# Performance work log

Hardware: AMD Instinct MI355X
Metric: run time of the kernel (lower is better)

The kernel has to match this reference:

```python
import jax, jax.numpy as jnp
import numpy as np

D_MODEL = 256
N_HEAD = 8


def quick_gelu(x):
    return x * jax.nn.sigmoid(1.702 * x)


def setup_inputs() -> dict:
    key = jax.random.key(0)
    ks = jax.random.split(key, 7)
    d = D_MODEL
    s = 0.02
    return {
        "x": jax.random.normal(ks[0], (2, 512, d), dtype=jnp.float32),
        "W_qkv": jax.random.normal(ks[1], (d, 3 * d), dtype=jnp.float32) * s,
        "b_qkv": jnp.zeros((3 * d,), dtype=jnp.float32),
        "W_fc": jax.random.normal(ks[2], (d, 4 * d), dtype=jnp.float32) * s,
        "b_fc": jnp.zeros((4 * d,), dtype=jnp.float32),
        "W_proj": jax.random.normal(ks[3], (4 * d, d), dtype=jnp.float32) * s,
        "b_proj": jnp.zeros((d,), dtype=jnp.float32),
    }


def attention_l1(x, W_qkv, b_qkv):
    bs, n_ctx, width = x.shape
    h = N_HEAD
    c = width // h
    scale = 1.0 / jnp.sqrt(jnp.asarray(c, x.dtype))
    qkv = (x @ W_qkv + b_qkv).reshape(bs, n_ctx, h, 3 * c)
    q, k, v = jnp.split(qkv, 3, axis=-1)  # each (b, t, h, c)
    qh = q.transpose(0, 2, 1, 3)  # (b, h, t, c)
    kh = k.transpose(0, 2, 1, 3)  # (b, h, s, c)
    vh = v.transpose(0, 2, 1, 3)  # (b, h, s, c)
    # L1 distance: sum_c |q - k| * scale  -> (b, h, t, s)
    dist = jnp.sum(jnp.abs(qh[:, :, :, None, :] - kh[:, :, None, :, :]), axis=-1) * scale
    weight = 1.0 / (0.001 + dist)
    idx = jnp.arange(n_ctx)
    weight = weight.at[:, :, idx, idx].set(0.0)
    wdtype = weight.dtype
    weight = jax.nn.softmax(weight.astype(jnp.float32), axis=-1).astype(wdtype)
    out = jnp.einsum('bhts,bhsc->bthc', weight, vh)
    return out.reshape(bs, n_ctx, width)


def reference(x, W_qkv, b_qkv, W_fc, b_fc, W_proj, b_proj):
    x = x + attention_l1(x, W_qkv, b_qkv)
    h = quick_gelu(x @ W_fc + b_fc)
    x = x + (h @ W_proj + b_proj)
    return x
```

## Files before the change

### kernel.cpp

```cpp
#include <hip/hip_runtime.h>
#include <hip/hip_bf16.h>
#include <hip/hip_fp16.h>

#define DM   256
#define NH   8
#define HC   32
#define SEQ  512
#define MTOT 1024

#define B_X1   0
#define B_QH   (1u<<20)
#define B_KH   0x180000u
#define B_VT   0x200000u
#define B_WFCT 0x280000u
#define B_WPJT 0x300000u

typedef __attribute__((ext_vector_type(8))) __bf16 bf16x8;
typedef __attribute__((ext_vector_type(4))) __bf16 bf16x4;
typedef __attribute__((ext_vector_type(4))) float  f32x4;

__device__ __forceinline__ float qgelu(float x) {
    return x / (1.0f + __expf(-1.702f * x));
}

#define BKP 264

__global__ __launch_bounds__(256)
void qkv_k(const float* __restrict__ x, const float* __restrict__ W,
           const float* __restrict__ bias,
           const float* __restrict__ Wfc, const float* __restrict__ Wproj,
           char* __restrict__ wsb)
{
    __shared__ float lt[64 * 65];
    __shared__ __align__(16) __bf16 lbt[16 * BKP];
    const int bid = blockIdx.x, tid = threadIdx.x;

    if (bid >= 768) {
        const int tt = bid - 768;
        const float* src; __bf16* dst; int K, N, tile;
        if (tt < 64) { src = Wfc;   dst = (__bf16*)(wsb + B_WFCT); K = 256;  N = 1024; tile = tt; }
        else         { src = Wproj; dst = (__bf16*)(wsb + B_WPJT); K = 1024; N = 256;  tile = tt - 64; }
        const int nn = N >> 6;
        const int k0 = (tile / nn) * 64, n0 = (tile % nn) * 64;
        const int rr0 = tid >> 4, c4 = tid & 15;
        #pragma unroll
        for (int i = 0; i < 4; ++i) {
            const int rr = rr0 + i * 16;
            float4 v = *(const float4*)&src[(size_t)(k0 + rr) * N + n0 + c4 * 4];
            lt[rr * 65 + c4 * 4 + 0] = v.x; lt[rr * 65 + c4 * 4 + 1] = v.y;
            lt[rr * 65 + c4 * 4 + 2] = v.z; lt[rr * 65 + c4 * 4 + 3] = v.w;
        }
        __syncthreads();
        #pragma unroll
        for (int i = 0; i < 4; ++i) {
            const int rr = rr0 + i * 16;
            bf16x4 b;
            b.x = (__bf16)lt[(c4 * 4 + 0) * 65 + rr];
            b.y = (__bf16)lt[(c4 * 4 + 1) * 65 + rr];
            b.z = (__bf16)lt[(c4 * 4 + 2) * 65 + rr];
            b.w = (__bf16)lt[(c4 * 4 + 3) * 65 + rr];
            *(bf16x4*)&dst[(size_t)(n0 + rr) * K + k0 + c4 * 4] = b;
        }
        return;
    }

    const int lane = tid & 63, wv = tid >> 6;
    const int n0 = (bid >> 4) * 16;
    const int m0 = ((bid * 4 + wv) & 63) * 16;
    const int r = lane & 15, q = lane >> 4;

    {
        const int kk = tid >> 2;
        const int c4 = (tid & 3) * 4;
        #pragma unroll
        for (int p = 0; p < 4; ++p) {
            const int k = p * 64 + kk;
            float4 w = *(const float4*)&W[(size_t)k * 768 + n0 + c4];
            lbt[(c4 + 0) * BKP + k] = (__bf16)w.x;
            lbt[(c4 + 1) * BKP + k] = (__bf16)w.y;
            lbt[(c4 + 2) * BKP + k] = (__bf16)w.z;
            lbt[(c4 + 3) * BKP + k] = (__bf16)w.w;
        }
    }
    __syncthreads();

    const float*  ap = x + (size_t)(m0 + r) * DM + q * 8;
    const __bf16* bl = &lbt[r * BKP + q * 8];

    f32x4 acc = {0.f, 0.f, 0.f, 0.f};
    #pragma unroll
    for (int kt = 0; kt < DM; kt += 32) {
        float4 a0 = *(const float4*)(ap + kt);
        float4 a1 = *(const float4*)(ap + kt + 4);
        bf16x8 af;
        af[0] = (__bf16)a0.x; af[1] = (__bf16)a0.y; af[2] = (__bf16)a0.z; af[3] = (__bf16)a0.w;
        af[4] = (__bf16)a1.x; af[5] = (__bf16)a1.y; af[6] = (__bf16)a1.z; af[7] = (__bf16)a1.w;
        bf16x8 bf = *(const bf16x8*)(bl + kt);
        acc = __builtin_amdgcn_mfma_f32_16x16x32_bf16(af, bf, acc, 0, 0, 0);
    }

    __half*  qh  = (__half*)(wsb + B_QH);
    __half*  kh  = (__half*)(wsb + B_KH);
    __bf16*  vtb = (__bf16*)(wsb + B_VT);
    const int n = n0 + r;
    const float bn = bias[n];
    const int h = n / 96, jj = n % 96;
    #pragma unroll
    for (int i = 0; i < 4; ++i) {
        const int m = m0 + q * 4 + i;
        const float v = acc[i] + bn;
        const int b = m >> 9, t = m & 511;
        const int bh = b * NH + h;
        if (jj < 32)      qh[((size_t)(bh * SEQ + t)) * HC + jj]        = (__half)v;
        else if (jj < 64) kh[((size_t)(bh * SEQ + t)) * HC + (jj - 32)] = (__half)v;
        else              vtb[((size_t)(bh * HC + (jj - 64))) * SEQ + t] = (__bf16)v;
    }
}

#define QT 16
#define PSTRIDE 514

__global__ __launch_bounds__(512, 4)
void attn_k(const char* __restrict__ wsb, const float* __restrict__ xin,
            float* __restrict__ x1, const float* __restrict__ bproj,
            float* __restrict__ out)
{
    __shared__ __half2 qtile[QT * 16];
    __shared__ __bf16  pmat[QT * PSTRIDE];
    __shared__ float   psum[QT * 8];
    __shared__ float   pinv[QT];

    const __half*  qhg = (const __half*)(wsb + B_QH);
    const __half*  khg = (const __half*)(wsb + B_KH);
    const __bf16*  vtb = (const __bf16*)(wsb + B_VT);

    const int tid  = threadIdx.x;
    const int lane = tid & 63;
    const int wv   = tid >> 6;
    const int sg   = tid;
    const int bh   = blockIdx.x >> 5;
    const int qbase = (blockIdx.x & 31) * QT;
    const float scale = 0.17677669529663687f;

    const __half2* kp = (const __half2*)(khg + ((size_t)(bh * SEQ + sg)) * HC);
    __half2 kr[16];
    #pragma unroll
    for (int j = 0; j < 16; ++j) kr[j] = kp[j];

    if (tid < 256) {
        const int t = tid >> 4, j = tid & 15;
        qtile[t * 16 + j] =
            *(const __half2*)(qhg + ((size_t)(bh * SEQ + qbase + t)) * HC + j * 2);
    }
    __syncthreads();

    #pragma unroll 4
    for (int t = 0; t < QT; ++t) {
        __half2 acc2 = __floats2half2_rn(0.f, 0.f);
        #pragma unroll
        for (int j = 0; j < 16; ++j) {
            __half2 dif = __hsub2(kr[j], qtile[t * 16 + j]);
            unsigned u = (*(unsigned*)&dif) & 0x7FFF7FFFu;
            acc2 = __hadd2(acc2, *(__half2*)&u);
        }
        const float d = __low2float(acc2) + __high2float(acc2);
        float w = 1.0f / (0.001f + d * scale);
        if (sg == qbase + t) w = 0.0f;
        float p = __expf(w);
        float se = p;
        #pragma unroll
        for (int off = 32; off >= 1; off >>= 1) se += __shfl_xor(se, off, 64);
        pmat[t * PSTRIDE + sg] = (__bf16)p;
        if (lane == 0) psum[t * 8 + wv] = se;
    }
    __syncthreads();

    if (tid < QT) {
        float s = 0.f;
        #pragma unroll
        for (int j = 0; j < 8; ++j) s += psum[tid * 8 + j];
        pinv[tid] = 1.0f / s;
    }
    __syncthreads();

    if (wv < 2) {
        const int r = lane & 15, q = lane >> 4;
        const __bf16* bp  = vtb + ((size_t)(bh * HC + wv * 16 + r)) * SEQ + q * 8;
        const __bf16* apm = &pmat[r * PSTRIDE + q * 8];
        f32x4 acc = {0.f, 0.f, 0.f, 0.f};
        #pragma unroll
        for (int kt = 0; kt < SEQ; kt += 32) {
            bf16x8 af = *(const bf16x8*)(apm + kt);
            bf16x8 bf = *(const bf16x8*)(bp + kt);
            acc = __builtin_amdgcn_mfma_f32_16x16x32_bf16(af, bf, acc, 0, 0, 0);
        }
        const int b = bh >> 3, hh = bh & 7;
        const int c = wv * 16 + r;
        const int col = hh * HC + c;
        const float bpn = bproj[col];
        #pragma unroll
        for (int i = 0; i < 4; ++i) {
            const int tl = q * 4 + i;
            const int t  = qbase + tl;
            const float v = acc[i] * pinv[tl];
            const int idx = ((b * SEQ + t) * DM) + col;
            const float res = xin[idx] + v;
            x1[idx]  = res;
            out[idx] = res + bpn;
        }
    }
}

#define HSTR 264

__global__ __launch_bounds__(512)
void mlp_k(const float* __restrict__ X1, const char* __restrict__ wsb,
           const float* __restrict__ bfc, float* __restrict__ out)
{
    __shared__ __align__(16) __bf16 hs[16 * HSTR];
    const __bf16* Wf = (const __bf16*)(wsb + B_WFCT);
    const __bf16* Wp = (const __bf16*)(wsb + B_WPJT);

    const int tid  = threadIdx.x;
    const int lane = tid & 63;
    const int wv   = tid >> 6;
    const int mt   = blockIdx.x & 63;
    const int ns   = blockIdx.x >> 6;
    const int m0   = mt * 16;
    const int r    = lane & 15, q = lane >> 4;

    {
        const float* ap = X1 + (size_t)(m0 + r) * DM + q * 8;
        f32x4 acc[2] = {};
        #pragma unroll
        for (int kt = 0; kt < DM; kt += 32) {
            float4 a0 = *(const float4*)(ap + kt);
            float4 a1 = *(const float4*)(ap + kt + 4);
            bf16x8 af;
            af[0] = (__bf16)a0.x; af[1] = (__bf16)a0.y; af[2] = (__bf16)a0.z; af[3] = (__bf16)a0.w;
            af[4] = (__bf16)a1.x; af[5] = (__bf16)a1.y; af[6] = (__bf16)a1.z; af[7] = (__bf16)a1.w;
            #pragma unroll
            for (int nt = 0; nt < 2; ++nt) {
                const int n0 = ns * 256 + (wv * 2 + nt) * 16;
                bf16x8 bf = *(const bf16x8*)(Wf + (size_t)(n0 + r) * DM + q * 8 + kt);
                acc[nt] = __builtin_amdgcn_mfma_f32_16x16x32_bf16(af, bf, acc[nt], 0, 0, 0);
            }
        }
        #pragma unroll
        for (int nt = 0; nt < 2; ++nt) {
            const int nl = (wv * 2 + nt) * 16 + r;
            const float bn = bfc[ns * 256 + nl];
            #pragma unroll
            for (int i = 0; i < 4; ++i)
                hs[(q * 4 + i) * HSTR + nl] = (__bf16)qgelu(acc[nt][i] + bn);
        }
    }
    __syncthreads();

    {
        f32x4 acc[2] = {};
        const __bf16* al = &hs[r * HSTR + q * 8];
        #pragma unroll
        for (int kt = 0; kt < 256; kt += 32) {
            bf16x8 af = *(const bf16x8*)(al + kt);
            #pragma unroll
            for (int nt = 0; nt < 2; ++nt) {
                const int n0 = wv * 32 + nt * 16;
                bf16x8 bf = *(const bf16x8*)(Wp + (size_t)(n0 + r) * 1024 +
                                             ns * 256 + q * 8 + kt);
                acc[nt] = __builtin_amdgcn_mfma_f32_16x16x32_bf16(af, bf, acc[nt], 0, 0, 0);
            }
        }
        #pragma unroll
        for (int nt = 0; nt < 2; ++nt) {
            const int n = wv * 32 + nt * 16 + r;
            #pragma unroll
            for (int i = 0; i < 4; ++i) {
                const int m = m0 + q * 4 + i;
                atomicAdd(&out[(size_t)m * DM + n], acc[nt][i]);
            }
        }
    }
}

extern "C" void kernel_launch(void* const* d_in, const int* in_sizes, int n_in,
                              void* d_out, int out_size, void* d_ws, size_t ws_size,
                              hipStream_t stream)
{
    (void)in_sizes; (void)n_in; (void)out_size; (void)ws_size;
    const float* x     = (const float*)d_in[0];
    const float* Wqkv  = (const float*)d_in[1];
    const float* bqkv  = (const float*)d_in[2];
    const float* Wfc   = (const float*)d_in[3];
    const float* bfc   = (const float*)d_in[4];
    const float* Wproj = (const float*)d_in[5];
    const float* bproj = (const float*)d_in[6];
    float* out = (float*)d_out;
    char*  wsb = (char*)d_ws;
    float* x1  = (float*)(wsb + B_X1);

    qkv_k<<<896, 256, 0, stream>>>(x, Wqkv, bqkv, Wfc, Wproj, wsb);

    attn_k<<<512, 512, 0, stream>>>(wsb, x, x1, bproj, out);

    mlp_k<<<256, 512, 0, stream>>>(x1, wsb, bfc, out);
}
```

Before: 106.8 us.

## Fuse QKV, attention and MLP kernels into one persistent kernel with grid barriers

Replaces three kernel launches with a single 256-block persistent kernel that runs the QKV GEMM and weight transposes, the L1 attention, and the MLP in phases. The phases are separated by atomic-counter grid barriers, and a memset resets the counter before each launch. Attention now handles 32 query rows per block instead of 16 so that 256 blocks cover the work. This removes launch gaps between kernels, but adds barrier spin cost, halves the number of attention blocks, and depends on all 256 blocks being co-resident.

```diff
diff --git a/kernel.cpp b/kernel.cpp
--- a/kernel.cpp
+++ b/kernel.cpp
@@ -14,6 +14,7 @@
 #define B_VT   0x200000u
 #define B_WFCT 0x280000u
 #define B_WPJT 0x300000u
+#define B_BAR  0x3C0000u
 
 typedef __attribute__((ext_vector_type(8))) __bf16 bf16x8;
 typedef __attribute__((ext_vector_type(4))) __bf16 bf16x4;
@@ -23,261 +24,283 @@
     return x / (1.0f + __expf(-1.702f * x));
 }
 
-#define BKP 264
-
-__global__ __launch_bounds__(256)
-void qkv_k(const float* __restrict__ x, const float* __restrict__ W,
-           const float* __restrict__ bias,
-           const float* __restrict__ Wfc, const float* __restrict__ Wproj,
-           char* __restrict__ wsb)
-{
-    __shared__ float lt[64 * 65];
-    __shared__ __align__(16) __bf16 lbt[16 * BKP];
-    const int bid = blockIdx.x, tid = threadIdx.x;
-
-    if (bid >= 768) {
-        const int tt = bid - 768;
-        const float* src; __bf16* dst; int K, N, tile;
-        if (tt < 64) { src = Wfc;   dst = (__bf16*)(wsb + B_WFCT); K = 256;  N = 1024; tile = tt; }
-        else         { src = Wproj; dst = (__bf16*)(wsb + B_WPJT); K = 1024; N = 256;  tile = tt - 64; }
-        const int nn = N >> 6;
-        const int k0 = (tile / nn) * 64, n0 = (tile % nn) * 64;
-        const int rr0 = tid >> 4, c4 = tid & 15;
-        #pragma unroll
-        for (int i = 0; i < 4; ++i) {
-            const int rr = rr0 + i * 16;
-            float4 v = *(const float4*)&src[(size_t)(k0 + rr) * N + n0 + c4 * 4];
-            lt[rr * 65 + c4 * 4 + 0] = v.x; lt[rr * 65 + c4 * 4 + 1] = v.y;
-            lt[rr * 65 + c4 * 4 + 2] = v.z; lt[rr * 65 + c4 * 4 + 3] = v.w;
-        }
-        __syncthreads();
-        #pragma unroll
-        for (int i = 0; i < 4; ++i) {
-            const int rr = rr0 + i * 16;
-            bf16x4 b;
-            b.x = (__bf16)lt[(c4 * 4 + 0) * 65 + rr];
-            b.y = (__bf16)lt[(c4 * 4 + 1) * 65 + rr];
-            b.z = (__bf16)lt[(c4 * 4 + 2) * 65 + rr];
-            b.w = (__bf16)lt[(c4 * 4 + 3) * 65 + rr];
-            *(bf16x4*)&dst[(size_t)(n0 + rr) * K + k0 + c4 * 4] = b;
-        }
-        return;
-    }
-
-    const int lane = tid & 63, wv = tid >> 6;
-    const int n0 = (bid >> 4) * 16;
-    const int m0 = ((bid * 4 + wv) & 63) * 16;
-    const int r = lane & 15, q = lane >> 4;
-
-    {
-        const int kk = tid >> 2;
-        const int c4 = (tid & 3) * 4;
-        #pragma unroll
-        for (int p = 0; p < 4; ++p) {
-            const int k = p * 64 + kk;
-            float4 w = *(const float4*)&W[(size_t)k * 768 + n0 + c4];
-            lbt[(c4 + 0) * BKP + k] = (__bf16)w.x;
-            lbt[(c4 + 1) * BKP + k] = (__bf16)w.y;
-            lbt[(c4 + 2) * BKP + k] = (__bf16)w.z;
-            lbt[(c4 + 3) * BKP + k] = (__bf16)w.w;
-        }
+#define NBLK    256
+#define BKP     264
+#define QT      32
+#define PSTRIDE 514
+#define HSTR    264
+
+__device__ __forceinline__ void gbar(unsigned* bar, unsigned target) {
+    __syncthreads();
+    if (threadIdx.x == 0) {
+        __threadfence();
+        __hip_atomic_fetch_add(bar, 1u, __ATOMIC_RELEASE, __HIP_MEMORY_SCOPE_AGENT);
+        while (__hip_atomic_load(bar, __ATOMIC_ACQUIRE, __HIP_MEMORY_SCOPE_AGENT) < target)
+            __builtin_amdgcn_s_sleep(2);
+        __threadfence();
     }
     __syncthreads();
-
-    const float*  ap = x + (size_t)(m0 + r) * DM + q * 8;
-    const __bf16* bl = &lbt[r * BKP + q * 8];
-
-    f32x4 acc = {0.f, 0.f, 0.f, 0.f};
-    #pragma unroll
-    for (int kt = 0; kt < DM; kt += 32) {
-        float4 a0 = *(const float4*)(ap + kt);
-        float4 a1 = *(const float4*)(ap + kt + 4);
-        bf16x8 af;
-        af[0] = (__bf16)a0.x; af[1] = (__bf16)a0.y; af[2] = (__bf16)a0.z; af[3] = (__bf16)a0.w;
-        af[4] = (__bf16)a1.x; af[5] = (__bf16)a1.y; af[6] = (__bf16)a1.z; af[7] = (__bf16)a1.w;
-        bf16x8 bf = *(const bf16x8*)(bl + kt);
-        acc = __builtin_amdgcn_mfma_f32_16x16x32_bf16(af, bf, acc, 0, 0, 0);
-    }
-
-    __half*  qh  = (__half*)(wsb + B_QH);
-    __half*  kh  = (__half*)(wsb + B_KH);
+}
+
+__global__ __launch_bounds__(512)
+void fused_k(const float* __restrict__ x, const float* __restrict__ W,
+             const float* __restrict__ bias,
+             const float* __restrict__ Wfc, const float* __restrict__ Wproj,
+             const float* __restrict__ bfc, const float* __restrict__ bproj,
+             char* __restrict__ wsb, float* __restrict__ out)
+{
+    __shared__ __align__(16) unsigned char SM[37 * 1024];
+    const int tid = threadIdx.x;
+    const int bid = blockIdx.x;
+    unsigned* bar = (unsigned*)(wsb + B_BAR);
+
+    float* x1 = (float*)(wsb + B_X1);
+    __half*  qhg = (__half*)(wsb + B_QH);
+    __half*  khg = (__half*)(wsb + B_KH);
     __bf16*  vtb = (__bf16*)(wsb + B_VT);
-    const int n = n0 + r;
-    const float bn = bias[n];
-    const int h = n / 96, jj = n % 96;
-    #pragma unroll
-    for (int i = 0; i < 4; ++i) {
-        const int m = m0 + q * 4 + i;
-        const float v = acc[i] + bn;
-        const int b = m >> 9, t = m & 511;
-        const int bh = b * NH + h;
-        if (jj < 32)      qh[((size_t)(bh * SEQ + t)) * HC + jj]        = (__half)v;
-        else if (jj < 64) kh[((size_t)(bh * SEQ + t)) * HC + (jj - 32)] = (__half)v;
-        else              vtb[((size_t)(bh * HC + (jj - 64))) * SEQ + t] = (__bf16)v;
-    }
-}
-
-#define QT 16
-#define PSTRIDE 514
-
-__global__ __launch_bounds__(512, 4)
-void attn_k(const char* __restrict__ wsb, const float* __restrict__ xin,
-            float* __restrict__ x1, const float* __restrict__ bproj,
-            float* __restrict__ out)
-{
-    __shared__ __half2 qtile[QT * 16];
-    __shared__ __bf16  pmat[QT * PSTRIDE];
-    __shared__ float   psum[QT * 8];
-    __shared__ float   pinv[QT];
-
-    const __half*  qhg = (const __half*)(wsb + B_QH);
-    const __half*  khg = (const __half*)(wsb + B_KH);
-    const __bf16*  vtb = (const __bf16*)(wsb + B_VT);
-
-    const int tid  = threadIdx.x;
-    const int lane = tid & 63;
-    const int wv   = tid >> 6;
-    const int sg   = tid;
-    const int bh   = blockIdx.x >> 5;
-    const int qbase = (blockIdx.x & 31) * QT;
-    const float scale = 0.17677669529663687f;
-
-    const __half2* kp = (const __half2*)(khg + ((size_t)(bh * SEQ + sg)) * HC);
-    __half2 kr[16];
-    #pragma unroll
-    for (int j = 0; j < 16; ++j) kr[j] = kp[j];
-
-    if (tid < 256) {
-        const int t = tid >> 4, j = tid & 15;
-        qtile[t * 16 + j] =
-            *(const __half2*)(qhg + ((size_t)(bh * SEQ + qbase + t)) * HC + j * 2);
-    }
-    __syncthreads();
-
-    #pragma unroll 4
-    for (int t = 0; t < QT; ++t) {
-        __half2 acc2 = __floats2half2_rn(0.f, 0.f);
-        #pragma unroll
-        for (int j = 0; j < 16; ++j) {
-            __half2 dif = __hsub2(kr[j], qtile[t * 16 + j]);
-            unsigned u = (*(unsigned*)&dif) & 0x7FFF7FFFu;
-            acc2 = __hadd2(acc2, *(__half2*)&u);
-        }
-        const float d = __low2float(acc2) + __high2float(acc2);
-        float w = 1.0f / (0.001f + d * scale);
-        if (sg == qbase + t) w = 0.0f;
-        float p = __expf(w);
-        float se = p;
-        #pragma unroll
-        for (int off = 32; off >= 1; off >>= 1) se += __shfl_xor(se, off, 64);
-        pmat[t * PSTRIDE + sg] = (__bf16)p;
-        if (lane == 0) psum[t * 8 + wv] = se;
-    }
-    __syncthreads();
-
-    if (tid < QT) {
-        float s = 0.f;
-        #pragma unroll
-        for (int j = 0; j < 8; ++j) s += psum[tid * 8 + j];
-        pinv[tid] = 1.0f / s;
-    }
-    __syncthreads();
-
-    if (wv < 2) {
-        const int r = lane & 15, q = lane >> 4;
-        const __bf16* bp  = vtb + ((size_t)(bh * HC + wv * 16 + r)) * SEQ + q * 8;
-        const __bf16* apm = &pmat[r * PSTRIDE + q * 8];
-        f32x4 acc = {0.f, 0.f, 0.f, 0.f};
-        #pragma unroll
-        for (int kt = 0; kt < SEQ; kt += 32) {
-            bf16x8 af = *(const bf16x8*)(apm + kt);
-            bf16x8 bf = *(const bf16x8*)(bp + kt);
-            acc = __builtin_amdgcn_mfma_f32_16x16x32_bf16(af, bf, acc, 0, 0, 0);
-        }
-        const int b = bh >> 3, hh = bh & 7;
-        const int c = wv * 16 + r;
-        const int col = hh * HC + c;
-        const float bpn = bproj[col];
-        #pragma unroll
-        for (int i = 0; i < 4; ++i) {
-            const int tl = q * 4 + i;
-            const int t  = qbase + tl;
-            const float v = acc[i] * pinv[tl];
-            const int idx = ((b * SEQ + t) * DM) + col;
-            const float res = xin[idx] + v;
-            x1[idx]  = res;
-            out[idx] = res + bpn;
-        }
-    }
-}
-
-#define HSTR 264
-
-__global__ __launch_bounds__(512)
-void mlp_k(const float* __restrict__ X1, const char* __restrict__ wsb,
-           const float* __restrict__ bfc, float* __restrict__ out)
-{
-    __shared__ __align__(16) __bf16 hs[16 * HSTR];
-    const __bf16* Wf = (const __bf16*)(wsb + B_WFCT);
-    const __bf16* Wp = (const __bf16*)(wsb + B_WPJT);
-
-    const int tid  = threadIdx.x;
-    const int lane = tid & 63;
-    const int wv   = tid >> 6;
-    const int mt   = blockIdx.x & 63;
-    const int ns   = blockIdx.x >> 6;
-    const int m0   = mt * 16;
-    const int r    = lane & 15, q = lane >> 4;
-
-    {
-        const float* ap = X1 + (size_t)(m0 + r) * DM + q * 8;
-        f32x4 acc[2] = {};
-        #pragma unroll
-        for (int kt = 0; kt < DM; kt += 32) {
-            float4 a0 = *(const float4*)(ap + kt);
-            float4 a1 = *(const float4*)(ap + kt + 4);
-            bf16x8 af;
-            af[0] = (__bf16)a0.x; af[1] = (__bf16)a0.y; af[2] = (__bf16)a0.z; af[3] = (__bf16)a0.w;
-            af[4] = (__bf16)a1.x; af[5] = (__bf16)a1.y; af[6] = (__bf16)a1.z; af[7] = (__bf16)a1.w;
-            #pragma unroll
-            for (int nt = 0; nt < 2; ++nt) {
-                const int n0 = ns * 256 + (wv * 2 + nt) * 16;
-                bf16x8 bf = *(const bf16x8*)(Wf + (size_t)(n0 + r) * DM + q * 8 + kt);
-                acc[nt] = __builtin_amdgcn_mfma_f32_16x16x32_bf16(af, bf, acc[nt], 0, 0, 0);
-            }
-        }
-        #pragma unroll
-        for (int nt = 0; nt < 2; ++nt) {
-            const int nl = (wv * 2 + nt) * 16 + r;
-            const float bn = bfc[ns * 256 + nl];
-            #pragma unroll
-            for (int i = 0; i < 4; ++i)
-                hs[(q * 4 + i) * HSTR + nl] = (__bf16)qgelu(acc[nt][i] + bn);
-        }
-    }
-    __syncthreads();
-
-    {
-        f32x4 acc[2] = {};
-        const __bf16* al = &hs[r * HSTR + q * 8];
-        #pragma unroll
-        for (int kt = 0; kt < 256; kt += 32) {
-            bf16x8 af = *(const bf16x8*)(al + kt);
-            #pragma unroll
-            for (int nt = 0; nt < 2; ++nt) {
-                const int n0 = wv * 32 + nt * 16;
-                bf16x8 bf = *(const bf16x8*)(Wp + (size_t)(n0 + r) * 1024 +
-                                             ns * 256 + q * 8 + kt);
-                acc[nt] = __builtin_amdgcn_mfma_f32_16x16x32_bf16(af, bf, acc[nt], 0, 0, 0);
-            }
-        }
-        #pragma unroll
-        for (int nt = 0; nt < 2; ++nt) {
-            const int n = wv * 32 + nt * 16 + r;
+
+    for (int pass = 0; pass < 2; ++pass) {
+        const int sub = tid >> 8;
+        const int vt  = tid & 255;
+        const int vb  = pass * 512 + bid * 2 + sub;
+        unsigned char* SB = SM + sub * 16640;
+        float*  lt  = (float*)SB;
+        __bf16* lbt = (__bf16*)SB;
+
+        const bool gemm = (vb < 768);
+        const bool tp   = (vb >= 768) && (vb < 896);
+
+        if (gemm) {
+            const int n0 = (vb >> 4) * 16;
+            const int kk = vt >> 2, c4 = (vt & 3) * 4;
+            #pragma unroll
+            for (int p = 0; p < 4; ++p) {
+                const int k = p * 64 + kk;
+                float4 w = *(const float4*)&W[(size_t)k * 768 + n0 + c4];
+                lbt[(c4 + 0) * BKP + k] = (__bf16)w.x;
+                lbt[(c4 + 1) * BKP + k] = (__bf16)w.y;
+                lbt[(c4 + 2) * BKP + k] = (__bf16)w.z;
+                lbt[(c4 + 3) * BKP + k] = (__bf16)w.w;
+            }
+        } else if (tp) {
+            const int tt = vb - 768;
+            const float* src; int K, N, tile;
+            if (tt < 64) { src = Wfc;   K = 256;  N = 1024; tile = tt; }
+            else         { src = Wproj; K = 1024; N = 256;  tile = tt - 64; }
+            const int nn = N >> 6;
+            const int k0 = (tile / nn) * 64, n0t = (tile % nn) * 64;
+            const int rr0 = vt >> 4, c4 = vt & 15;
+            #pragma unroll
+            for (int i = 0; i < 4; ++i) {
+                const int rr = rr0 + i * 16;
+                float4 v = *(const float4*)&src[(size_t)(k0 + rr) * N + n0t + c4 * 4];
+                lt[rr * 65 + c4 * 4 + 0] = v.x; lt[rr * 65 + c4 * 4 + 1] = v.y;
+                lt[rr * 65 + c4 * 4 + 2] = v.z; lt[rr * 65 + c4 * 4 + 3] = v.w;
+            }
+        }
+        __syncthreads();
+
+        if (gemm) {
+            const int lane = vt & 63, wv = vt >> 6;
+            const int n0 = (vb >> 4) * 16;
+            const int m0 = ((vb * 4 + wv) & 63) * 16;
+            const int r = lane & 15, q = lane >> 4;
+            const float*  ap = x + (size_t)(m0 + r) * DM + q * 8;
+            const __bf16* bl = &lbt[r * BKP + q * 8];
+            f32x4 acc = {0.f, 0.f, 0.f, 0.f};
+            #pragma unroll
+            for (int kt = 0; kt < DM; kt += 32) {
+                float4 a0 = *(const float4*)(ap + kt);
+                float4 a1 = *(const float4*)(ap + kt + 4);
+                bf16x8 af;
+                af[0] = (__bf16)a0.x; af[1] = (__bf16)a0.y; af[2] = (__bf16)a0.z; af[3] = (__bf16)a0.w;
+                af[4] = (__bf16)a1.x; af[5] = (__bf16)a1.y; af[6] = (__bf16)a1.z; af[7] = (__bf16)a1.w;
+                bf16x8 bf = *(const bf16x8*)(bl + kt);
+                acc = __builtin_amdgcn_mfma_f32_16x16x32_bf16(af, bf, acc, 0, 0, 0);
+            }
+            const int n = n0 + r;
+            const float bn = bias[n];
+            const int h = n / 96, jj = n % 96;
             #pragma unroll
             for (int i = 0; i < 4; ++i) {
                 const int m = m0 + q * 4 + i;
-                atomicAdd(&out[(size_t)m * DM + n], acc[nt][i]);
+                const float v = acc[i] + bn;
+                const int b = m >> 9, t = m & 511;
+                const int bh = b * NH + h;
+                if (jj < 32)      qhg[((size_t)(bh * SEQ + t)) * HC + jj]        = (__half)v;
+                else if (jj < 64) khg[((size_t)(bh * SEQ + t)) * HC + (jj - 32)] = (__half)v;
+                else              vtb[((size_t)(bh * HC + (jj - 64))) * SEQ + t] = (__bf16)v;
+            }
+        } else if (tp) {
+            const int tt = vb - 768;
+            __bf16* dst; int K, N, tile;
+            if (tt < 64) { dst = (__bf16*)(wsb + B_WFCT); K = 256;  N = 1024; tile = tt; }
+            else         { dst = (__bf16*)(wsb + B_WPJT); K = 1024; N = 256;  tile = tt - 64; }
+            const int nn = N >> 6;
+            const int k0 = (tile / nn) * 64, n0t = (tile % nn) * 64;
+            const int rr0 = vt >> 4, c4 = vt & 15;
+            #pragma unroll
+            for (int i = 0; i < 4; ++i) {
+                const int rr = rr0 + i * 16;
+                bf16x4 bv;
+                bv.x = (__bf16)lt[(c4 * 4 + 0) * 65 + rr];
+                bv.y = (__bf16)lt[(c4 * 4 + 1) * 65 + rr];
+                bv.z = (__bf16)lt[(c4 * 4 + 2) * 65 + rr];
+                bv.w = (__bf16)lt[(c4 * 4 + 3) * 65 + rr];
+                *(bf16x4*)&dst[(size_t)(n0t + rr) * K + k0 + c4 * 4] = bv;
+            }
+        }
+        __syncthreads();
+    }
+
+    gbar(bar, NBLK);
+
+    {
+        __bf16*  pmat  = (__bf16*)SM;
+        __half2* qtile = (__half2*)(SM + 32896);
+        float*   psum  = (float*)(SM + 34944);
+        float*   pinv  = (float*)(SM + 35968);
+
+        const int lane = tid & 63;
+        const int wv   = tid >> 6;
+        const int sg   = tid;
+        const int bh   = bid >> 4;
+        const int qbase = (bid & 15) * QT;
+        const float scale = 0.17677669529663687f;
+
+        const __half2* kp = (const __half2*)(khg + ((size_t)(bh * SEQ + sg)) * HC);
+        __half2 kr[16];
+        #pragma unroll
+        for (int j = 0; j < 16; ++j) kr[j] = kp[j];
+
+        {
+            const int t = tid >> 4, j = tid & 15;
+            qtile[t * 16 + j] =
+                *(const __half2*)(qhg + ((size_t)(bh * SEQ + qbase + t)) * HC + j * 2);
+        }
+        __syncthreads();
+
+        #pragma unroll 4
+        for (int t = 0; t < QT; ++t) {
+            __half2 acc2 = __floats2half2_rn(0.f, 0.f);
+            #pragma unroll
+            for (int j = 0; j < 16; ++j) {
+                __half2 dif = __hsub2(kr[j], qtile[t * 16 + j]);
+                unsigned u = (*(unsigned*)&dif) & 0x7FFF7FFFu;
+                acc2 = __hadd2(acc2, *(__half2*)&u);
+            }
+            const float d = __low2float(acc2) + __high2float(acc2);
+            float w = 1.0f / (0.001f + d * scale);
+            if (sg == qbase + t) w = 0.0f;
+            float p = __expf(w);
+            float se = p;
+            #pragma unroll
+            for (int off = 32; off >= 1; off >>= 1) se += __shfl_xor(se, off, 64);
+            pmat[t * PSTRIDE + sg] = (__bf16)p;
+            if (lane == 0) psum[t * 8 + wv] = se;
+        }
+        __syncthreads();
+
+        if (tid < QT) {
+            float s = 0.f;
+            #pragma unroll
+            for (int j = 0; j < 8; ++j) s += psum[tid * 8 + j];
+            pinv[tid] = 1.0f / s;
+        }
+        __syncthreads();
+
+        if (wv < 4) {
+            const int mq = wv >> 1, nc = wv & 1;
+            const int r = lane & 15, q = lane >> 4;
+            const __bf16* bp  = vtb + ((size_t)(bh * HC + nc * 16 + r)) * SEQ + q * 8;
+            const __bf16* apm = &pmat[(mq * 16 + r) * PSTRIDE + q * 8];
+            f32x4 acc = {0.f, 0.f, 0.f, 0.f};
+            #pragma unroll
+            for (int kt = 0; kt < SEQ; kt += 32) {
+                bf16x8 af = *(const bf16x8*)(apm + kt);
+                bf16x8 bf = *(const bf16x8*)(bp + kt);
+                acc = __builtin_amdgcn_mfma_f32_16x16x32_bf16(af, bf, acc, 0, 0, 0);
+            }
+            const int b = bh >> 3, hh = bh & 7;
+            const int col = hh * HC + nc * 16 + r;
+            const float bpn = bproj[col];
+            #pragma unroll
+            for (int i = 0; i < 4; ++i) {
+                const int tl = mq * 16 + q * 4 + i;
+                const int t  = qbase + tl;
+                const float v = acc[i] * pinv[tl];
+                const int idx = ((b * SEQ + t) * DM) + col;
+                const float res = x[idx] + v;
+                x1[idx]  = res;
+                out[idx] = res + bpn;
+            }
+        }
+    }
+
+    gbar(bar, 2 * NBLK);
+
+    {
+        __bf16* hs = (__bf16*)SM;
+        const __bf16* Wf = (const __bf16*)(wsb + B_WFCT);
+        const __bf16* Wp = (const __bf16*)(wsb + B_WPJT);
+
+        const int lane = tid & 63;
+        const int wv   = tid >> 6;
+        const int mt   = bid & 63;
+        const int ns   = bid >> 6;
+        const int m0   = mt * 16;
+        const int r    = lane & 15, q = lane >> 4;
+
+        {
+            const float* ap = x1 + (size_t)(m0 + r) * DM + q * 8;
+            f32x4 acc[2] = {};
+            #pragma unroll
+            for (int kt = 0; kt < DM; kt += 32) {
+                float4 a0 = *(const float4*)(ap + kt);
+                float4 a1 = *(const float4*)(ap + kt + 4);
+                bf16x8 af;
+                af[0] = (__bf16)a0.x; af[1] = (__bf16)a0.y; af[2] = (__bf16)a0.z; af[3] = (__bf16)a0.w;
+                af[4] = (__bf16)a1.x; af[5] = (__bf16)a1.y; af[6] = (__bf16)a1.z; af[7] = (__bf16)a1.w;
+                #pragma unroll
+                for (int nt = 0; nt < 2; ++nt) {
+                    const int n0 = ns * 256 + (wv * 2 + nt) * 16;
+                    bf16x8 bf = *(const bf16x8*)(Wf + (size_t)(n0 + r) * DM + q * 8 + kt);
+                    acc[nt] = __builtin_amdgcn_mfma_f32_16x16x32_bf16(af, bf, acc[nt], 0, 0, 0);
+                }
+            }
+            #pragma unroll
+            for (int nt = 0; nt < 2; ++nt) {
+                const int nl = (wv * 2 + nt) * 16 + r;
+                const float bn = bfc[ns * 256 + nl];
+                #pragma unroll
+                for (int i = 0; i < 4; ++i)
+                    hs[(q * 4 + i) * HSTR + nl] = (__bf16)qgelu(acc[nt][i] + bn);
+            }
+        }
+        __syncthreads();
+
+        {
+            f32x4 acc[2] = {};
+            const __bf16* al = &hs[r * HSTR + q * 8];
+            #pragma unroll
+            for (int kt = 0; kt < 256; kt += 32) {
+                bf16x8 af = *(const bf16x8*)(al + kt);
+                #pragma unroll
+                for (int nt = 0; nt < 2; ++nt) {
+                    const int n0 = wv * 32 + nt * 16;
+                    bf16x8 bf = *(const bf16x8*)(Wp + (size_t)(n0 + r) * 1024 +
+                                                 ns * 256 + q * 8 + kt);
+                    acc[nt] = __builtin_amdgcn_mfma_f32_16x16x32_bf16(af, bf, acc[nt], 0, 0, 0);
+                }
+            }
+            #pragma unroll
+            for (int nt = 0; nt < 2; ++nt) {
+                const int n = wv * 32 + nt * 16 + r;
+                #pragma unroll
+                for (int i = 0; i < 4; ++i) {
+                    const int m = m0 + q * 4 + i;
+                    atomicAdd(&out[(size_t)m * DM + n], acc[nt][i]);
+                }
             }
         }
     }
@@ -297,11 +320,8 @@
     const float* bproj = (const float*)d_in[6];
     float* out = (float*)d_out;
     char*  wsb = (char*)d_ws;
-    float* x1  = (float*)(wsb + B_X1);
-
-    qkv_k<<<896, 256, 0, stream>>>(x, Wqkv, bqkv, Wfc, Wproj, wsb);
-
-    attn_k<<<512, 512, 0, stream>>>(wsb, x, x1, bproj, out);
-
-    mlp_k<<<256, 512, 0, stream>>>(x1, wsb, bfc, out);
+
+    hipMemsetAsync(wsb + B_BAR, 0, 64, stream);
+    fused_k<<<NBLK, 512, 0, stream>>>(x, Wqkv, bqkv, Wfc, Wproj,
+                                      bfc, bproj, wsb, out);
 }
```

Result: slower. 180.5 us (+69.1%).
